# Kernel optimization log

Hardware: AMD Instinct MI355X
Metric: run time of the kernel (lower is better)

Reference implementation:

```python
import jax, jax.numpy as jnp
import numpy as np

B, T, C, HS = 4, 4096, 1024, 128

def setup_inputs() -> dict:
    key = jax.random.key(0)
    kx, kk, kq, kv = jax.random.split(key, 4)
    x = jax.random.normal(kx, (B, T, C), dtype=jnp.float32)
    # torch Linear(n_embd, head_size, bias=False): y = x @ W.T with W [hs, C].
    # We store the transposed form W [C, hs] so y = x @ W (same math).
    s = C ** -0.5  # kaiming-ish scale to keep activations sane
    Wk = jax.random.normal(kk, (C, HS), dtype=jnp.float32) * s
    Wq = jax.random.normal(kq, (C, HS), dtype=jnp.float32) * s
    Wv = jax.random.normal(kv, (C, HS), dtype=jnp.float32) * s
    return {"x": x, "Wk": Wk, "Wq": Wq, "Wv": Wv}

def reference(x, Wk, Wq, Wv):
    # Single causal self-attention head (dropout = identity, eval mode).
    k = jnp.einsum('btc,ch->bth', x, Wk)  # [B,T,hs]
    q = jnp.einsum('btc,ch->bth', x, Wq)
    v = jnp.einsum('btc,ch->bth', x, Wv)
    scale = k.shape[-1] ** -0.5
    wei = jnp.einsum('bqh,bkh->bqk', q, k) * scale  # [B,T,T]
    Tq = x.shape[1]
    causal = jnp.tril(jnp.ones((Tq, Tq), dtype=bool))
    wei = jnp.where(causal, wei, -jnp.inf)
    wei = jax.nn.softmax(wei, axis=-1)
    out = jnp.einsum('bqk,bkh->bqh', wei, v)  # [B,T,hs]
    return out
```

## Files before the change

### kernel.cpp

```cpp
#include <hip/hip_runtime.h>
#include <hip/hip_bf16.h>
#include <math.h>

#define B_  4
#define T_  4096
#define C_  1024
#define HS_ 128

using bf16x8 = __attribute__((ext_vector_type(8))) __bf16;
using bf16x4 = __attribute__((ext_vector_type(4))) __bf16;
using f32x4  = __attribute__((ext_vector_type(4))) float;

#define MFMA(a, b, c) __builtin_amdgcn_mfma_f32_16x16x32_bf16(a, b, c, 0, 0, 0)

typedef __attribute__((address_space(1))) const float gfloat;
typedef __attribute__((address_space(3))) float lfloat;

__device__ inline float fexp2(float x) {
  float r;
  asm volatile("v_exp_f32 %0, %1\n\ts_nop 0" : "=v"(r) : "v"(x));
  return r;
}


__global__ __launch_bounds__(256) void prep_w_kernel(
    const float* __restrict__ Wk, const float* __restrict__ Wq,
    const float* __restrict__ Wv, __bf16* __restrict__ Wt) {
  const int m  = blockIdx.x >> 4;
  const int k0 = (blockIdx.x & 15) * 64;
  const float* W = (m == 0) ? Wq : ((m == 1) ? Wk : Wv);
  const float scale = (m == 0) ? (0.08838834764831845f * 1.4426950408889634f) : 1.0f;
  __shared__ __bf16 tile[128][72];
  const int t = threadIdx.x;
#pragma unroll
  for (int p = 0; p < 8; ++p) {
    int e  = p * 1024 + t * 4;
    int r  = e >> 7;
    int cc = e & 127;
    float4 w = *reinterpret_cast<const float4*>(&W[(size_t)(k0 + r) * HS_ + cc]);
    tile[cc + 0][r] = (__bf16)(w.x * scale);
    tile[cc + 1][r] = (__bf16)(w.y * scale);
    tile[cc + 2][r] = (__bf16)(w.z * scale);
    tile[cc + 3][r] = (__bf16)(w.w * scale);
  }
  __syncthreads();
#pragma unroll
  for (int p = 0; p < 4; ++p) {
    int e  = p * 2048 + t * 8;
    int n  = e >> 6;
    int kk = e & 63;
    bf16x8 v;
#pragma unroll
    for (int jj = 0; jj < 8; ++jj) v[jj] = tile[n][kk + jj];
    *reinterpret_cast<bf16x8*>(&Wt[((size_t)m * 128 + n) * C_ + k0 + kk]) = v;
  }
}

__device__ inline bf16x8 cvt8p(float4 u, float4 v) {
  bf16x8 r;
  r[0] = (__bf16)u.x; r[1] = (__bf16)u.y; r[2] = (__bf16)u.z; r[3] = (__bf16)u.w;
  r[4] = (__bf16)v.x; r[5] = (__bf16)v.y; r[6] = (__bf16)v.z; r[7] = (__bf16)v.w;
  return r;
}

__global__ __launch_bounds__(512) void proj_kernel(
    const float* __restrict__ x, const __bf16* __restrict__ Wt,
    __bf16* __restrict__ Qf, __bf16* __restrict__ Kf, __bf16* __restrict__ Vf) {
  __shared__ __align__(16) char lds[98304];
  const int tid = threadIdx.x;
  const int wid = tid >> 6;
  const int l   = tid & 63;
  const int c   = l & 15;
  const int g   = l >> 4;
  const int wr  = wid >> 2;
  const int wc  = wid & 3;
  const int rbase = blockIdx.x * 64;

  f32x4 acc[6][2];
#pragma unroll
  for (int i = 0; i < 6; ++i) { acc[i][0] = 0.f; acc[i][1] = 0.f; }

  const int xrow = tid >> 3;
  const int xch  = tid & 7;
  const float* xsrc = x + (size_t)(rbase + xrow) * C_ + ((xch ^ (xrow & 7)) << 2);
  const __bf16* wsrc[3];
  int wdst[3];
#pragma unroll
  for (int i = 0; i < 3; ++i) {
    int id2 = i * 512 + tid;
    int cg  = id2 >> 2;
    int kc  = id2 & 3;
    wsrc[i] = Wt + (size_t)cg * C_ + ((kc ^ (cg & 3)) << 3);
    wdst[i] = 8192 + id2 * 16;
  }

  auto stage = [&](int t, int bo) {
    __builtin_amdgcn_global_load_lds((gfloat*)(xsrc + t * 32),
        (lfloat*)(lds + bo + tid * 16), 16, 0, 0);
#pragma unroll
    for (int i = 0; i < 3; ++i)
      __builtin_amdgcn_global_load_lds((gfloat*)(wsrc[i] + t * 32),
          (lfloat*)(lds + bo + wdst[i]), 16, 0, 0);
  };

  int woffs[6];
#pragma unroll
  for (int i = 0; i < 6; ++i) {
    int u  = wc * 6 + i;
    int cg = (u >> 3) * 128 + (u & 7) * 16 + c;
    woffs[i] = 8192 + cg * 64 + ((g ^ (cg & 3)) << 4);
  }
  int xoffs[2][2];
#pragma unroll
  for (int rt = 0; rt < 2; ++rt) {
    int row = wr * 32 + rt * 16 + c;
#pragma unroll
    for (int j = 0; j < 2; ++j)
      xoffs[rt][j] = row * 128 + ((((g << 1) | j) ^ (row & 7)) << 4);
  }

  stage(0, 0);
  stage(1, 32768);
  asm volatile("s_waitcnt vmcnt(4)" ::: "memory");
  __syncthreads();

  int b0 = 0, b1 = 32768, b2 = 65536;
  for (int t = 0; t < 32; ++t) {
    const bool more = (t + 2 < 32);
    if (more) stage(t + 2, b2);

    bf16x8 wf[6];
#pragma unroll
    for (int i = 0; i < 6; ++i)
      wf[i] = *reinterpret_cast<const bf16x8*>(lds + b0 + woffs[i]);
#pragma unroll
    for (int rt = 0; rt < 2; ++rt) {
      float4 lo = *reinterpret_cast<const float4*>(lds + b0 + xoffs[rt][0]);
      float4 hi = *reinterpret_cast<const float4*>(lds + b0 + xoffs[rt][1]);
      bf16x8 a = cvt8p(lo, hi);
#pragma unroll
      for (int i = 0; i < 6; ++i) acc[i][rt] = MFMA(a, wf[i], acc[i][rt]);
    }

    if (more) {
      asm volatile("s_waitcnt vmcnt(4)" ::: "memory");
    } else {
      asm volatile("s_waitcnt vmcnt(0)" ::: "memory");
    }
    __syncthreads();
    int tmp = b0; b0 = b1; b1 = b2; b2 = tmp;
  }

  const size_t tile2 = (size_t)blockIdx.x * 2 + wr;
#pragma unroll
  for (int i = 0; i < 6; ++i) {
    const int u = wc * 6 + i;
    const int m = u >> 3, nt = u & 7;
    const int gprime = ((nt & 1) << 1) + (c >> 3);
    const int e = c & 7;
    if (m == 0) {
#pragma unroll
      for (int rt = 0; rt < 2; ++rt)
#pragma unroll
        for (int rr = 0; rr < 4; ++rr)
          Qf[(tile2 * 8 + rt * 4 + (nt >> 1)) * 512 +
             (gprime * 16 + 4 * g + rr) * 8 + e] = (__bf16)acc[i][rt][rr];
    } else if (m == 1) {
#pragma unroll
      for (int rt = 0; rt < 2; ++rt)
#pragma unroll
        for (int rr = 0; rr < 4; ++rr)
          Kf[(tile2 * 8 + 2 * (nt >> 1) + (g & 1)) * 512 +
             (gprime * 16 + (((2 * rt + (g >> 1)) << 2) | rr)) * 8 + e] =
              (__bf16)acc[i][rt][rr];
    } else {
#pragma unroll
      for (int rt = 0; rt < 2; ++rt) {
        bf16x4 v4;
#pragma unroll
        for (int rr = 0; rr < 4; ++rr) v4[rr] = (__bf16)acc[i][rt][rr];
        *reinterpret_cast<bf16x4*>(
            Vf + (tile2 * 8 + nt) * 512 +
            ((2 * rt + (g >> 1)) * 16 + c) * 8 + 4 * (g & 1)) = v4;
      }
    }
  }
}

__global__ __launch_bounds__(256, 2) void attn_kernel(
    const __bf16* __restrict__ Qf, const __bf16* __restrict__ Kf,
    const __bf16* __restrict__ Vf, float* __restrict__ out) {
  __shared__ float sm[4][32];
  __shared__ float sl[4][32];
  __shared__ float bufA[32][132];
  __shared__ float bufB[32][132];

  const int tid = threadIdx.x;
  const int wid = tid >> 6;
  const int l   = tid & 63;
  const int c   = l & 15;
  const int g   = l >> 4;
  const int bid = blockIdx.x;
  const int b   = (bid & 7) >> 1;
  const int j   = ((bid >> 3) << 1) | (bid & 1);
  const int qt  = (j < 64) ? (127 - j) : (j - 64);
  const int qb  = qt * 32;

  bf16x8 qf[2][4];
  {
    const __bf16* Qt = Qf + (size_t)(b * 128 + qt) * 4096 + l * 8;
#pragma unroll
    for (int rt = 0; rt < 2; ++rt)
#pragma unroll
      for (int cs = 0; cs < 4; ++cs)
        qf[rt][cs] = *reinterpret_cast<const bf16x8*>(Qt + (rt * 4 + cs) * 512);
  }

  f32x4 acc[2][8];
#pragma unroll
  for (int i = 0; i < 2; ++i)
#pragma unroll
    for (int d = 0; d < 8; ++d) acc[i][d] = 0.f;
  float mrun[2] = {-INFINITY, -INFINITY};
  float lrun[2] = {0.f, 0.f};

  if (wid <= qt) {
    const __bf16* Kb8 = Kf + (size_t)b * 128 * 4096 + l * 8;
    const __bf16* Vb8 = Vf + (size_t)b * 128 * 4096 + l * 8;
    bf16x8 kreg[8];
    auto kload = [&](int kt) {
      const __bf16* kb = Kb8 + (size_t)kt * 4096;
#pragma unroll
      for (int jj = 0; jj < 8; ++jj)
        kreg[jj] = *reinterpret_cast<const bf16x8*>(kb + jj * 512);
    };
    kload(wid);

    for (int kt = wid; kt <= qt; kt += 4) {
      f32x4 s00 = 0.f, s01 = 0.f, s10 = 0.f, s11 = 0.f;
      __builtin_amdgcn_s_setprio(1);
#pragma unroll
      for (int cs = 0; cs < 4; ++cs) {
        s00 = MFMA(kreg[2 * cs], qf[0][cs], s00);
        s01 = MFMA(kreg[2 * cs + 1], qf[0][cs], s01);
        s10 = MFMA(kreg[2 * cs], qf[1][cs], s10);
        s11 = MFMA(kreg[2 * cs + 1], qf[1][cs], s11);
      }
      __builtin_amdgcn_s_setprio(0);

      bf16x8 vf[8];
      {
        const __bf16* vb = Vb8 + (size_t)kt * 4096;
#pragma unroll
        for (int db = 0; db < 8; ++db)
          vf[db] = *reinterpret_cast<const bf16x8*>(vb + db * 512);
      }

      if (kt + 4 <= qt) kload(kt + 4);

      const bool maskt = (kt == qt);
      bf16x8 pb[2];
#pragma unroll
      for (int rt = 0; rt < 2; ++rt) {
        float p[8];
        const f32x4 sa = rt ? s10 : s00;
        const f32x4 sb = rt ? s11 : s01;
#pragma unroll
        for (int rr = 0; rr < 4; ++rr) { p[rr] = sa[rr]; p[4 + rr] = sb[rr]; }
        if (maskt) {
          const int lim = rt * 16 + c;
#pragma unroll
          for (int jj = 0; jj < 8; ++jj)
            if (8 * g + jj > lim) p[jj] = -INFINITY;
        }
        float t0 = fmaxf(fmaxf(p[0], p[1]), p[2]);
        float t1 = fmaxf(fmaxf(p[3], p[4]), p[5]);
        float t2 = fmaxf(fmaxf(p[6], p[7]), t0);
        float tmax = fmaxf(t1, t2);

        if (!__all(tmax <= mrun[rt] + 11.5415603f)) {
          float cmax = fmaxf(tmax, __shfl_xor(tmax, 16));
          cmax = fmaxf(cmax, __shfl_xor(cmax, 32));
          float mnew = fmaxf(mrun[rt], cmax);
          float al   = fexp2(mrun[rt] - mnew);
          mrun[rt] = mnew;
          lrun[rt] *= al;
#pragma unroll
          for (int db = 0; db < 8; ++db) acc[rt][db] *= al;
        }
        const float mc = mrun[rt];
#pragma unroll
        for (int jj = 0; jj < 8; ++jj) p[jj] = fexp2(p[jj] - mc);
        lrun[rt] += ((p[0] + p[1]) + (p[2] + p[3])) + ((p[4] + p[5]) + (p[6] + p[7]));
#pragma unroll
        for (int jj = 0; jj < 8; ++jj) pb[rt][jj] = (__bf16)p[jj];
      }

      __builtin_amdgcn_s_setprio(1);
#pragma unroll
      for (int db = 0; db < 8; ++db) {
        acc[0][db] = MFMA(vf[db], pb[0], acc[0][db]);
        acc[1][db] = MFMA(vf[db], pb[1], acc[1][db]);
      }
      __builtin_amdgcn_s_setprio(0);
    }
  }

#pragma unroll
  for (int rt = 0; rt < 2; ++rt) {
    lrun[rt] += __shfl_xor(lrun[rt], 16);
    lrun[rt] += __shfl_xor(lrun[rt], 32);
  }

  if (g == 0) {
    sm[wid][c] = mrun[0]; sm[wid][16 + c] = mrun[1];
    sl[wid][c] = lrun[0]; sl[wid][16 + c] = lrun[1];
  }
  __syncthreads();

  float linv[2];
#pragma unroll
  for (int rt = 0; rt < 2; ++rt) {
    const int q = rt * 16 + c;
    float ms = fmaxf(fmaxf(sm[0][q], sm[1][q]), fmaxf(sm[2][q], sm[3][q]));
    float ls = fexp2(sm[0][q] - ms) * sl[0][q] + fexp2(sm[1][q] - ms) * sl[1][q]
             + fexp2(sm[2][q] - ms) * sl[2][q] + fexp2(sm[3][q] - ms) * sl[3][q];
    float al = fexp2(mrun[rt] - ms);
#pragma unroll
    for (int db = 0; db < 8; ++db) acc[rt][db] *= al;
    linv[rt] = 1.0f / ls;
  }

  auto store_buf = [&](float(*buf)[132]) {
#pragma unroll
    for (int rt = 0; rt < 2; ++rt)
#pragma unroll
      for (int db = 0; db < 8; ++db)
        *reinterpret_cast<f32x4*>(&buf[rt * 16 + c][db * 16 + 4 * g]) = acc[rt][db];
  };
  auto add_buf = [&](float(*buf)[132]) {
#pragma unroll
    for (int rt = 0; rt < 2; ++rt)
#pragma unroll
      for (int db = 0; db < 8; ++db)
        acc[rt][db] += *reinterpret_cast<const f32x4*>(&buf[rt * 16 + c][db * 16 + 4 * g]);
  };

  if (wid == 2) store_buf(bufA);
  if (wid == 3) store_buf(bufB);
  __syncthreads();
  if (wid == 0) add_buf(bufA);
  if (wid == 1) add_buf(bufB);
  __syncthreads();
  if (wid == 1) store_buf(bufA);
  __syncthreads();
  if (wid == 0) {
    add_buf(bufA);
    float* op = out + ((size_t)b * T_ + qb) * HS_;
#pragma unroll
    for (int rt = 0; rt < 2; ++rt)
#pragma unroll
      for (int db = 0; db < 8; ++db) {
        f32x4 v = acc[rt][db] * linv[rt];
        *reinterpret_cast<f32x4*>(op + (size_t)(rt * 16 + c) * HS_ + db * 16 + 4 * g) = v;
      }
  }
}

extern "C" void kernel_launch(void* const* d_in, const int* in_sizes, int n_in,
                              void* d_out, int out_size, void* d_ws, size_t ws_size,
                              hipStream_t stream) {
  const float* x  = (const float*)d_in[0];
  const float* Wk = (const float*)d_in[1];
  const float* Wq = (const float*)d_in[2];
  const float* Wv = (const float*)d_in[3];
  float* out = (float*)d_out;

  char* ws = (char*)d_ws;
  __bf16* Wt = (__bf16*)ws;
  __bf16* Qf = (__bf16*)(ws + 786432);
  __bf16* Kf = (__bf16*)(ws + 786432 + 4194304);
  __bf16* Vf = (__bf16*)(ws + 786432 + 8388608);

  prep_w_kernel<<<48, 256, 0, stream>>>(Wk, Wq, Wv, Wt);
  proj_kernel<<<256, 512, 0, stream>>>(x, Wt, Qf, Kf, Vf);
  attn_kernel<<<512, 256, 0, stream>>>(Qf, Kf, Vf, out);
}
```

Measured before the change: 73.64 us.

## Split projection into 32-row blocks with double buffering

Each projection block now covers 32 rows of x instead of 64, with 256 threads and 512 blocks, so the grid fills more CUs on the 256-CU device. The triple-buffered pipeline becomes a double buffer with a full vmcnt(0) wait every iteration, which shrinks LDS per block and may allow more resident blocks. The cost is that every block reloads the whole weight tile, doubling weight traffic per row, and prefetch depth drops from two stages to one.

```diff
diff --git a/kernel.cpp b/kernel.cpp
--- a/kernel.cpp
+++ b/kernel.cpp
@@ -63,18 +63,16 @@
   return r;
 }
 
-__global__ __launch_bounds__(512) void proj_kernel(
+__global__ __launch_bounds__(256) void proj_kernel(
     const float* __restrict__ x, const __bf16* __restrict__ Wt,
     __bf16* __restrict__ Qf, __bf16* __restrict__ Kf, __bf16* __restrict__ Vf) {
-  __shared__ __align__(16) char lds[98304];
+  __shared__ __align__(16) char lds[57344];
   const int tid = threadIdx.x;
   const int wid = tid >> 6;
   const int l   = tid & 63;
   const int c   = l & 15;
   const int g   = l >> 4;
-  const int wr  = wid >> 2;
-  const int wc  = wid & 3;
-  const int rbase = blockIdx.x * 64;
+  const int rbase = blockIdx.x * 32;
 
   f32x4 acc[6][2];
 #pragma unroll
@@ -83,78 +81,69 @@
   const int xrow = tid >> 3;
   const int xch  = tid & 7;
   const float* xsrc = x + (size_t)(rbase + xrow) * C_ + ((xch ^ (xrow & 7)) << 2);
-  const __bf16* wsrc[3];
-  int wdst[3];
-#pragma unroll
-  for (int i = 0; i < 3; ++i) {
-    int id2 = i * 512 + tid;
+  const __bf16* wsrc[6];
+#pragma unroll
+  for (int i = 0; i < 6; ++i) {
+    int id2 = i * 256 + tid;
     int cg  = id2 >> 2;
     int kc  = id2 & 3;
     wsrc[i] = Wt + (size_t)cg * C_ + ((kc ^ (cg & 3)) << 3);
-    wdst[i] = 8192 + id2 * 16;
   }
 
   auto stage = [&](int t, int bo) {
     __builtin_amdgcn_global_load_lds((gfloat*)(xsrc + t * 32),
         (lfloat*)(lds + bo + tid * 16), 16, 0, 0);
 #pragma unroll
-    for (int i = 0; i < 3; ++i)
+    for (int i = 0; i < 6; ++i)
       __builtin_amdgcn_global_load_lds((gfloat*)(wsrc[i] + t * 32),
-          (lfloat*)(lds + bo + wdst[i]), 16, 0, 0);
+          (lfloat*)(lds + bo + 4096 + (i * 256 + tid) * 16), 16, 0, 0);
   };
 
   int woffs[6];
 #pragma unroll
   for (int i = 0; i < 6; ++i) {
-    int u  = wc * 6 + i;
+    int u  = wid * 6 + i;
     int cg = (u >> 3) * 128 + (u & 7) * 16 + c;
-    woffs[i] = 8192 + cg * 64 + ((g ^ (cg & 3)) << 4);
+    woffs[i] = 4096 + cg * 64 + ((g ^ (cg & 3)) << 4);
   }
   int xoffs[2][2];
 #pragma unroll
   for (int rt = 0; rt < 2; ++rt) {
-    int row = wr * 32 + rt * 16 + c;
+    int row = rt * 16 + c;
 #pragma unroll
     for (int j = 0; j < 2; ++j)
       xoffs[rt][j] = row * 128 + ((((g << 1) | j) ^ (row & 7)) << 4);
   }
 
   stage(0, 0);
-  stage(1, 32768);
-  asm volatile("s_waitcnt vmcnt(4)" ::: "memory");
-  __syncthreads();
-
-  int b0 = 0, b1 = 32768, b2 = 65536;
+  asm volatile("s_waitcnt vmcnt(0)" ::: "memory");
+  __syncthreads();
+
   for (int t = 0; t < 32; ++t) {
-    const bool more = (t + 2 < 32);
-    if (more) stage(t + 2, b2);
+    const int bo = (t & 1) * 28672;
+    if (t + 1 < 32) stage(t + 1, bo ^ 28672);
 
     bf16x8 wf[6];
 #pragma unroll
     for (int i = 0; i < 6; ++i)
-      wf[i] = *reinterpret_cast<const bf16x8*>(lds + b0 + woffs[i]);
+      wf[i] = *reinterpret_cast<const bf16x8*>(lds + bo + woffs[i]);
 #pragma unroll
     for (int rt = 0; rt < 2; ++rt) {
-      float4 lo = *reinterpret_cast<const float4*>(lds + b0 + xoffs[rt][0]);
-      float4 hi = *reinterpret_cast<const float4*>(lds + b0 + xoffs[rt][1]);
+      float4 lo = *reinterpret_cast<const float4*>(lds + bo + xoffs[rt][0]);
+      float4 hi = *reinterpret_cast<const float4*>(lds + bo + xoffs[rt][1]);
       bf16x8 a = cvt8p(lo, hi);
 #pragma unroll
       for (int i = 0; i < 6; ++i) acc[i][rt] = MFMA(a, wf[i], acc[i][rt]);
     }
 
-    if (more) {
-      asm volatile("s_waitcnt vmcnt(4)" ::: "memory");
-    } else {
-      asm volatile("s_waitcnt vmcnt(0)" ::: "memory");
-    }
+    asm volatile("s_waitcnt vmcnt(0)" ::: "memory");
     __syncthreads();
-    int tmp = b0; b0 = b1; b1 = b2; b2 = tmp;
-  }
-
-  const size_t tile2 = (size_t)blockIdx.x * 2 + wr;
+  }
+
+  const size_t tile = blockIdx.x;
 #pragma unroll
   for (int i = 0; i < 6; ++i) {
-    const int u = wc * 6 + i;
+    const int u = wid * 6 + i;
     const int m = u >> 3, nt = u & 7;
     const int gprime = ((nt & 1) << 1) + (c >> 3);
     const int e = c & 7;
@@ -163,14 +152,14 @@
       for (int rt = 0; rt < 2; ++rt)
 #pragma unroll
         for (int rr = 0; rr < 4; ++rr)
-          Qf[(tile2 * 8 + rt * 4 + (nt >> 1)) * 512 +
+          Qf[(tile * 8 + rt * 4 + (nt >> 1)) * 512 +
              (gprime * 16 + 4 * g + rr) * 8 + e] = (__bf16)acc[i][rt][rr];
     } else if (m == 1) {
 #pragma unroll
       for (int rt = 0; rt < 2; ++rt)
 #pragma unroll
         for (int rr = 0; rr < 4; ++rr)
-          Kf[(tile2 * 8 + 2 * (nt >> 1) + (g & 1)) * 512 +
+          Kf[(tile * 8 + 2 * (nt >> 1) + (g & 1)) * 512 +
              (gprime * 16 + (((2 * rt + (g >> 1)) << 2) | rr)) * 8 + e] =
               (__bf16)acc[i][rt][rr];
     } else {
@@ -180,7 +169,7 @@
 #pragma unroll
         for (int rr = 0; rr < 4; ++rr) v4[rr] = (__bf16)acc[i][rt][rr];
         *reinterpret_cast<bf16x4*>(
-            Vf + (tile2 * 8 + nt) * 512 +
+            Vf + (tile * 8 + nt) * 512 +
             ((2 * rt + (g >> 1)) * 16 + c) * 8 + 4 * (g & 1)) = v4;
       }
     }
@@ -383,6 +372,6 @@
   __bf16* Vf = (__bf16*)(ws + 786432 + 8388608);
 
   prep_w_kernel<<<48, 256, 0, stream>>>(Wk, Wq, Wv, Wt);
-  proj_kernel<<<256, 512, 0, stream>>>(x, Wt, Qf, Kf, Vf);
+  proj_kernel<<<512, 256, 0, stream>>>(x, Wt, Qf, Kf, Vf);
   attn_kernel<<<512, 256, 0, stream>>>(Qf, Kf, Vf, out);
 }
```

Result: no change. 72.42 us (-1.7%).
